# Kernel tuning notes

Measured on AMD Instinct MI355X. Metric: run time of the kernel, lower is better.

Reference implementation:

```python
import jax, jax.numpy as jnp
import numpy as np
from jax import lax

BATCH = 32; SEQ_LEN = 336; ENC_IN = 7; MARK_IN = 4
D_MODEL = 512; D_FF = 2048; N_HEADS = 8; DK = 64; DV = 64
E_LAYERS = 3; D_BOTTLE = 128; PRED_LEN = 96
WINDOW = (4, 4, 4); INNER = 5


def _mask_sizes():
    # Pyraformer get_mask: True = masked out
    all_size = [SEQ_LEN]
    for w in WINDOW:
        all_size.append(all_size[-1] // w)
    S = sum(all_size)
    m = np.zeros((S, S), bool)  # True = may attend
    iw = INNER // 2
    starts = np.cumsum([0] + all_size)
    for l, sz in enumerate(all_size):
        st = int(starts[l])
        for i in range(st, st + sz):
            m[i, max(i - iw, st):min(i + iw + 1, st + sz)] = True
    for l in range(1, len(all_size)):
        st = int(starts[l])
        for i in range(st, st + all_size[l]):
            left = (st - all_size[l - 1]) + (i - st) * WINDOW[l - 1]
            right = st if i == st + all_size[l] - 1 else (st - all_size[l - 1]) + (i - st + 1) * WINDOW[l - 1]
            m[i, left:right] = True
            m[left:right, i] = True
    return ~m, all_size


def _refer_points(all_size):
    idx = np.zeros((all_size[0], len(all_size)), np.int64)
    for i in range(all_size[0]):
        idx[i, 0] = i
        former = i
        for j in range(1, len(all_size)):
            start = sum(all_size[:j])
            inner = former - (start - all_size[j - 1])
            former = start + min(inner // WINDOW[j - 1], all_size[j] - 1)
            idx[i, j] = former
    return idx


def _pos_enc(L, d):
    pos = np.arange(L)[:, None].astype(np.float32)
    div = np.exp(np.arange(0, d, 2).astype(np.float32) * (-np.log(10000.0) / d))
    pe = np.zeros((L, d), np.float32)
    pe[:, 0::2] = np.sin(pos * div)
    pe[:, 1::2] = np.cos(pos * div)
    return pe


def _ln(x, g, b, eps=1e-5):
    mu = jnp.mean(x, -1, keepdims=True)
    v = jnp.mean((x - mu) ** 2, -1, keepdims=True)
    return (x - mu) * lax.rsqrt(v + eps) * g + b


def setup_inputs():
    key = jax.random.key(0)
    ks = iter(jax.random.split(key, 64))
    def nrm(shape, s=0.02):
        return jax.random.normal(next(ks), shape, jnp.float32) * s
    mask, all_size = _mask_sizes()
    inp = {
        "x_enc": jax.random.normal(next(ks), (BATCH, SEQ_LEN, ENC_IN), jnp.float32),
        "x_mark_enc": jax.random.normal(next(ks), (BATCH, SEQ_LEN, MARK_IN), jnp.float32),
        "x_dec": jax.random.normal(next(ks), (BATCH, PRED_LEN, ENC_IN), jnp.float32),
        "x_mark_dec": jax.random.normal(next(ks), (BATCH, PRED_LEN, MARK_IN), jnp.float32),
        "conv_embed_w": nrm((D_MODEL, ENC_IN, 3), 0.1),
        "time_w": nrm((MARK_IN, D_MODEL)),
        "time_b": jnp.zeros((D_MODEL,), jnp.float32),
        "down_w": nrm((D_MODEL, D_BOTTLE)),
        "down_b": jnp.zeros((D_BOTTLE,), jnp.float32),
        "cscm_conv_w": nrm((3, D_BOTTLE, D_BOTTLE, 4), 0.05),
        "cscm_conv_b": jnp.zeros((3, D_BOTTLE), jnp.float32),
        "bn_g": jnp.ones((3, D_BOTTLE), jnp.float32),
        "bn_b": jnp.zeros((3, D_BOTTLE), jnp.float32),
        "up_w": nrm((D_BOTTLE, D_MODEL)),
        "up_b": jnp.zeros((D_MODEL,), jnp.float32),
        "cscm_ln_g": jnp.ones((D_MODEL,), jnp.float32),
        "cscm_ln_b": jnp.zeros((D_MODEL,), jnp.float32),
        "wq": nrm((E_LAYERS, D_MODEL, N_HEADS * DK)),
        "wk": nrm((E_LAYERS, D_MODEL, N_HEADS * DK)),
        "wv": nrm((E_LAYERS, D_MODEL, N_HEADS * DV)),
        "wo": nrm((E_LAYERS, N_HEADS * DV, D_MODEL)),
        "ln1_g": jnp.ones((E_LAYERS, D_MODEL), jnp.float32),
        "ln1_b": jnp.zeros((E_LAYERS, D_MODEL), jnp.float32),
        "ffn_w1": nrm((E_LAYERS, D_MODEL, D_FF)),
        "ffn_b1": jnp.zeros((E_LAYERS, D_FF), jnp.float32),
        "ffn_w2": nrm((E_LAYERS, D_FF, D_MODEL)),
        "ffn_b2": jnp.zeros((E_LAYERS, D_MODEL), jnp.float32),
        "ln2_g": jnp.ones((E_LAYERS, D_MODEL), jnp.float32),
        "ln2_b": jnp.zeros((E_LAYERS, D_MODEL), jnp.float32),
        "pred_w": nrm((len(all_size) * D_MODEL, PRED_LEN * ENC_IN)),
        "attn_mask": jnp.asarray(mask),                 # [S,S] bool, True = masked
        "indexes": jnp.asarray(_refer_points(all_size)),  # [336, 4] int64
    }
    return inp


def _forward(x_enc, x_mark_enc, conv_embed_w, time_w, time_b, down_w, down_b,
             cscm_conv_w, cscm_conv_b, bn_g, bn_b, up_w, up_b, cscm_ln_g, cscm_ln_b,
             wq, wk, wv, wo, ln1_g, ln1_b, ffn_w1, ffn_b1, ffn_w2, ffn_b2, ln2_g, ln2_b,
             pred_w, attn_mask, indexes):
    B = x_enc.shape[0]
    dn = ('NWC', 'OIW', 'NWC')
    # DataEmbedding: circular conv1d token embedding + sinusoidal pos + linear time-feature embedding
    xp = jnp.concatenate([x_enc[:, -1:], x_enc, x_enc[:, :1]], axis=1)  # circular pad, k=3
    tok = lax.conv_general_dilated(xp, conv_embed_w, (1,), 'VALID', dimension_numbers=dn)
    pe = jnp.asarray(_pos_enc(SEQ_LEN, D_MODEL))
    emb = tok + pe[None] + x_mark_enc @ time_w + time_b  # [B,336,512]
    # Bottleneck_Construct (CSCM): down-proj, strided convs per scale, up-proj, concat, LN
    x = emb @ down_w + down_b  # [B,336,128]
    outs = []
    for i in range(len(WINDOW)):
        x = lax.conv_general_dilated(x, cscm_conv_w[i], (WINDOW[i],), 'VALID', dimension_numbers=dn) + cscm_conv_b[i]
        x = x * bn_g[i] + bn_b[i]  # eval-mode BatchNorm1d (running mean 0 / var 1)
        x = jax.nn.elu(x)
        outs.append(x)  # lengths 84, 21, 5
    coarse = jnp.concatenate(outs, axis=1) @ up_w + up_b  # [B,110,512]
    seq = _ln(jnp.concatenate([emb, coarse], axis=1), cscm_ln_g, cscm_ln_b)  # [B,446,512]
    S = seq.shape[1]
    neg = jnp.where(attn_mask, jnp.float32(-1e9), jnp.float32(0.0))  # [S,S]
    scale = 1.0 / np.sqrt(DK).astype(np.float32)
    for l in range(E_LAYERS):  # post-norm encoder layers
        q = (seq @ wq[l]).reshape(B, S, N_HEADS, DK)
        k = (seq @ wk[l]).reshape(B, S, N_HEADS, DK)
        v = (seq @ wv[l]).reshape(B, S, N_HEADS, DV)
        attn = jax.nn.softmax(jnp.einsum('bihd,bjhd->bhij', q, k) * scale + neg, axis=-1)
        o = jnp.einsum('bhij,bjhd->bihd', attn, v).reshape(B, S, N_HEADS * DV)
        seq = _ln(seq + o @ wo[l], ln1_g[l], ln1_b[l])
        h = jax.nn.gelu(seq @ ffn_w1[l] + ffn_b1[l], approximate=False)
        seq = _ln(seq + h @ ffn_w2[l] + ffn_b2[l], ln2_g[l], ln2_b[l])
    # pyramidal readout: gather each scale's ancestor node for every fine position
    g = seq[:, indexes.reshape(-1), :].reshape(B, SEQ_LEN, -1)  # [B,336,4*512]
    enc_out = g[:, -1, :]  # [B,2048]
    return (enc_out @ pred_w).reshape(B, PRED_LEN, ENC_IN)


def reference(x_enc, x_mark_enc, x_dec, x_mark_dec, conv_embed_w, time_w, time_b,
              down_w, down_b, cscm_conv_w, cscm_conv_b, bn_g, bn_b, up_w, up_b,
              cscm_ln_g, cscm_ln_b, wq, wk, wv, wo, ln1_g, ln1_b, ffn_w1, ffn_b1,
              ffn_w2, ffn_b2, ln2_g, ln2_b, pred_w, attn_mask, indexes):
    # x_dec / x_mark_dec are unused by Pyraformer's forward (kept for signature parity)
    return _forward(x_enc, x_mark_enc, conv_embed_w, time_w, time_b, down_w, down_b,
                    cscm_conv_w, cscm_conv_b, bn_g, bn_b, up_w, up_b, cscm_ln_g, cscm_ln_b,
                    wq, wk, wv, wo, ln1_g, ln1_b, ffn_w1, ffn_b1, ffn_w2, ffn_b2,
                    ln2_g, ln2_b, pred_w, attn_mask, indexes)
```

## Files before the change

kernel.cpp:

```cpp
#include <hip/hip_runtime.h>
#include <math.h>

constexpr int BB   = 32;
constexpr int L    = 336;
constexpr int CIN  = 7;
constexpr int MARK = 4;
constexpr int D    = 512;
constexpr int DFF  = 2048;
constexpr int NH   = 8;
constexpr int HD   = 64;
constexpr int S    = 446;
constexpr int DBOT = 128;
constexpr int L1 = 84, L2 = 21, L3 = 5;
constexpr int LC = 110;
constexpr int NLAYER = 3;
constexpr int PRED_N = 672;
constexpr int MP   = 14336;
constexpr int NMAX = 12;
constexpr int MCONV1 = BB * L1;
constexpr int MCONV2P = 768;
constexpr int MCAT  = 3584;

using short8  = __attribute__((ext_vector_type(8))) short;
using float4v = __attribute__((ext_vector_type(4))) float;

struct SetsData {
    int nbr[S][NMAX];
    int idx[4][S];
    int cnt[4];
};

constexpr SetsData compute_sets() {
    SetsData sd{};
    constexpr int sizes[4]  = {336, 84, 21, 5};
    constexpr int starts[4] = {0, 336, 420, 441};
    for (int i = 0; i < S; ++i) {
        int li = 0, pi = i;
        if (i < 336)      { li = 0; pi = i; }
        else if (i < 420) { li = 1; pi = i - 336; }
        else if (i < 441) { li = 2; pi = i - 420; }
        else              { li = 3; pi = i - 441; }
        int cnt = 0;
        for (int d = -2; d <= 2; ++d) {
            int q = pi + d;
            if (q >= 0 && q < sizes[li]) sd.nbr[i][cnt++] = starts[li] + q;
        }
        if (li > 0) {
            int lo = pi * 4;
            int hi = (pi == sizes[li] - 1) ? sizes[li - 1] : (pi + 1) * 4;
            for (int c = lo; c < hi; ++c) sd.nbr[i][cnt++] = starts[li - 1] + c;
        }
        if (li < 3) {
            int q = pi >> 2;
            if (q > sizes[li + 1] - 1) q = sizes[li + 1] - 1;
            sd.nbr[i][cnt++] = starts[li + 1] + q;
        }
        for (int j = cnt; j < NMAX; ++j) sd.nbr[i][j] = -1;
    }
    sd.cnt[3] = 4;
    sd.idx[3][0] = 335; sd.idx[3][1] = 419; sd.idx[3][2] = 440; sd.idx[3][3] = 445;
    for (int lvl = 3; lvl >= 1; --lvl) {
        bool mk[S] = {};
        for (int k = 0; k < sd.cnt[lvl]; ++k) {
            int i = sd.idx[lvl][k];
            for (int t = 0; t < NMAX; ++t) {
                int v = sd.nbr[i][t];
                if (v >= 0) mk[v] = true;
            }
        }
        int nc = 0;
        for (int i = 0; i < S; ++i)
            if (mk[i]) sd.idx[lvl - 1][nc++] = i;
        sd.cnt[lvl - 1] = nc;
    }
    return sd;
}

constexpr SetsData HS = compute_sets();
__constant__ SetsData d_sets = compute_sets();

constexpr size_t psk_elems() {
    size_t mx = 0;
    for (int l = 0; l < NLAYER; ++l) {
        size_t Mc = (size_t)HS.cnt[l + 1] * 32;
        size_t Mpad = ((Mc + 127) / 128) * 128;
        if (Mc <= 512) { size_t v = 4 * Mpad * 512;  if (v > mx) mx = v; }
        if (Mc <= 128) { size_t v = 4 * Mpad * 2048; if (v > mx) mx = v; }
        size_t ks = (Mc <= 512) ? 8 : 4;
        size_t v = ks * Mpad * 512; if (v > mx) mx = v;
    }
    return mx;
}

__device__ inline short f2bf(float f) {
    union { float f; unsigned u; } v; v.f = f;
    unsigned r = v.u + 0x7fffu + ((v.u >> 16) & 1u);
    return (short)(r >> 16);
}
__device__ inline float bf2f(short h) {
    union { unsigned u; float f; } v; v.u = ((unsigned)(unsigned short)h) << 16;
    return v.f;
}

__device__ inline void gload_lds16(const void* g, void* l) {
    __builtin_amdgcn_global_load_lds(
        (const __attribute__((address_space(1))) void*)g,
        (__attribute__((address_space(3))) void*)l, 16, 0, 0);
}


template<int EPI>
__launch_bounds__(256, 4)
__global__ void mfma_gemm(const short* __restrict__ A, const short* __restrict__ Bt,
                          const float* __restrict__ bias, const float* __restrict__ bias2,
                          void* __restrict__ Cout, int Kd, int Nd,
                          int alvl, int clvl, int cnt,
                          const float* __restrict__ peT, short* __restrict__ Cout2) {
    __shared__ short As[2][128 * 32];
    __shared__ short Bs[2][128 * 32];
    int tid = threadIdx.x;
    int nwg  = gridDim.x * gridDim.y;
    int orig = blockIdx.y * gridDim.x + blockIdx.x;
    int qq = nwg >> 3, rr = nwg & 7;
    int xcd = orig & 7, idx = orig >> 3;
    int wgid = (xcd < rr ? xcd * (qq + 1) : rr * (qq + 1) + (xcd - rr) * qq) + idx;
    int m0 = (wgid / gridDim.x) * 128, n0 = (wgid % gridDim.x) * 128;

    int lane = tid & 63, wid = tid >> 6;
    int wm = wid >> 1, wn = wid & 1;
    int lr = lane & 15, lk = lane >> 4;

    size_t abase[2], bbase[2];
#pragma unroll
    for (int r = 0; r < 2; ++r) {
        int u = r * 256 + tid;
        int row = ((u >> 3) << 1) | ((u >> 2) & 1);
        int kg  = (u & 3) ^ ((u >> 3) & 3);
        int rm = m0 + row, ga;
        if (alvl >= 0) { int j = rm >> 5; if (j > cnt - 1) j = cnt - 1; ga = (rm & 31) * S + d_sets.idx[alvl][j]; }
        else ga = rm;
        abase[r] = (size_t)ga * Kd + kg * 8;
        bbase[r] = (size_t)(n0 + row) * Kd + kg * 8;
    }
    auto stage = [&](int buf, int k0) {
#pragma unroll
        for (int r = 0; r < 2; ++r) {
            short* la = As[buf] + (size_t)(r * 256 + wid * 64) * 8;
            short* lb = Bs[buf] + (size_t)(r * 256 + wid * 64) * 8;
            gload_lds16(A + abase[r] + k0, la);
            gload_lds16(Bt + bbase[r] + k0, lb);
        }
    };
    auto rd_off = [&](int row_) {
        int rh = row_ >> 1;
        int s  = lk ^ (rh & 3);
        return (size_t)(rh * 8 + (row_ & 1) * 4 + s) * 8;
    };

    float4v acc[4][4];
#pragma unroll
    for (int i = 0; i < 4; ++i)
#pragma unroll
        for (int j = 0; j < 4; ++j) acc[i][j] = 0;

    const int nt = Kd >> 5;
    stage(0, 0);
    for (int t = 0; t < nt; ++t) {
        int cur = t & 1;
        if (t + 1 < nt) {
            stage(cur ^ 1, (t + 1) * 32);
            asm volatile("s_waitcnt vmcnt(4)" ::: "memory");
        } else {
            asm volatile("s_waitcnt vmcnt(0)" ::: "memory");
        }
        __builtin_amdgcn_s_barrier();
        short8 af[4], bfv[4];
#pragma unroll
        for (int mi = 0; mi < 4; ++mi)
            af[mi] = *(const short8*)(As[cur] + rd_off(wm * 64 + mi * 16 + lr));
#pragma unroll
        for (int ni = 0; ni < 4; ++ni)
            bfv[ni] = *(const short8*)(Bs[cur] + rd_off(wn * 64 + ni * 16 + lr));
        __builtin_amdgcn_s_setprio(1);
#pragma unroll
        for (int mi = 0; mi < 4; ++mi)
#pragma unroll
            for (int ni = 0; ni < 4; ++ni)
                acc[mi][ni] = __builtin_amdgcn_mfma_f32_16x16x32_bf16(
                    af[mi], bfv[ni], acc[mi][ni], 0, 0, 0);
        __builtin_amdgcn_s_setprio(0);
        __builtin_amdgcn_s_barrier();
    }

#pragma unroll
    for (int mi = 0; mi < 4; ++mi) {
        int gmc = m0 + wm * 64 + mi * 16 + lk * 4;
#pragma unroll
        for (int ni = 0; ni < 4; ++ni) {
            int gn = n0 + wn * 64 + ni * 16 + lr;
            float bsv = (EPI == 1 || EPI == 3 || EPI == 4) ? bias[gn] : 0.0f;
            float sc = (EPI == 5) ? bias[gn]  : 0.0f;
            float sh = (EPI == 5) ? bias2[gn] : 0.0f;
#pragma unroll
            for (int e = 0; e < 4; ++e) {
                int rm = gmc + e, grow;
                if (clvl >= 0) { int j = rm >> 5; if (j > cnt - 1) j = cnt - 1; grow = (rm & 31) * S + d_sets.idx[clvl][j]; }
                else grow = rm;
                float v = acc[mi][ni][e] + bsv;
                if (EPI == 3) v = 0.5f * v * (1.0f + erff(v * 0.70710678118654752f));
                if (EPI == 5) { v = v * sc + sh; v = v > 0.0f ? v : (expf(v) - 1.0f); }
                if (EPI == 6) {
                    v += peT[(size_t)(grow % L) * D + gn];
                    ((float*)Cout)[(size_t)grow * Nd + gn] = v;
                    Cout2[(size_t)grow * Nd + gn] = f2bf(v);
                } else if (EPI <= 1) {
                    ((float*)Cout)[(size_t)grow * Nd + gn] = v;
                } else {
                    ((short*)Cout)[(size_t)grow * Nd + gn] = f2bf(v);
                }
            }
        }
    }
}

__launch_bounds__(256, 4)
__global__ void mfma_gemm_sk(const short* __restrict__ A, const short* __restrict__ Bt,
                             float* __restrict__ part, int Kd, int Nd,
                             int alvl, int cnt) {
    __shared__ short As[2][128 * 32];
    __shared__ short Bs[2][128 * 32];
    int tid = threadIdx.x;
    int nwg  = gridDim.x * gridDim.y;
    int orig = blockIdx.y * gridDim.x + blockIdx.x;
    int qq = nwg >> 3, rr = nwg & 7;
    int xcd = orig & 7, idx = orig >> 3;
    int wgid = (xcd < rr ? xcd * (qq + 1) : rr * (qq + 1) + (xcd - rr) * qq) + idx;
    int m0 = (wgid / gridDim.x) * 128, n0 = (wgid % gridDim.x) * 128;
    int Mpad = gridDim.y * 128;
    int kz = blockIdx.z;
    int kb = Kd / gridDim.z;
    int kbase = kz * kb;

    int lane = tid & 63, wid = tid >> 6;
    int wm = wid >> 1, wn = wid & 1;
    int lr = lane & 15, lk = lane >> 4;

    size_t abase[2], bbase[2];
#pragma unroll
    for (int r = 0; r < 2; ++r) {
        int u = r * 256 + tid;
        int row = ((u >> 3) << 1) | ((u >> 2) & 1);
        int kg  = (u & 3) ^ ((u >> 3) & 3);
        int rm = m0 + row, ga;
        if (alvl >= 0) { int j = rm >> 5; if (j > cnt - 1) j = cnt - 1; ga = (rm & 31) * S + d_sets.idx[alvl][j]; }
        else ga = rm;
        abase[r] = (size_t)ga * Kd + kbase + kg * 8;
        bbase[r] = (size_t)(n0 + row) * Kd + kbase + kg * 8;
    }
    auto stage = [&](int buf, int k0) {
#pragma unroll
        for (int r = 0; r < 2; ++r) {
            short* la = As[buf] + (size_t)(r * 256 + wid * 64) * 8;
            short* lb = Bs[buf] + (size_t)(r * 256 + wid * 64) * 8;
            gload_lds16(A + abase[r] + k0, la);
            gload_lds16(Bt + bbase[r] + k0, lb);
        }
    };
    auto rd_off = [&](int row_) {
        int rh = row_ >> 1;
        int s  = lk ^ (rh & 3);
        return (size_t)(rh * 8 + (row_ & 1) * 4 + s) * 8;
    };

    float4v acc[4][4];
#pragma unroll
    for (int i = 0; i < 4; ++i)
#pragma unroll
        for (int j = 0; j < 4; ++j) acc[i][j] = 0;

    const int nt = kb >> 5;
    stage(0, 0);
    for (int t = 0; t < nt; ++t) {
        int cur = t & 1;
        if (t + 1 < nt) {
            stage(cur ^ 1, (t + 1) * 32);
            asm volatile("s_waitcnt vmcnt(4)" ::: "memory");
        } else {
            asm volatile("s_waitcnt vmcnt(0)" ::: "memory");
        }
        __builtin_amdgcn_s_barrier();
        short8 af[4], bfv[4];
#pragma unroll
        for (int mi = 0; mi < 4; ++mi)
            af[mi] = *(const short8*)(As[cur] + rd_off(wm * 64 + mi * 16 + lr));
#pragma unroll
        for (int ni = 0; ni < 4; ++ni)
            bfv[ni] = *(const short8*)(Bs[cur] + rd_off(wn * 64 + ni * 16 + lr));
        __builtin_amdgcn_s_setprio(1);
#pragma unroll
        for (int mi = 0; mi < 4; ++mi)
#pragma unroll
            for (int ni = 0; ni < 4; ++ni)
                acc[mi][ni] = __builtin_amdgcn_mfma_f32_16x16x32_bf16(
                    af[mi], bfv[ni], acc[mi][ni], 0, 0, 0);
        __builtin_amdgcn_s_setprio(0);
        __builtin_amdgcn_s_barrier();
    }

#pragma unroll
    for (int mi = 0; mi < 4; ++mi) {
        int gmc = m0 + wm * 64 + mi * 16 + lk * 4;
#pragma unroll
        for (int ni = 0; ni < 4; ++ni) {
            int gn = n0 + wn * 64 + ni * 16 + lr;
#pragma unroll
            for (int e = 0; e < 4; ++e)
                part[((size_t)kz * Mpad + gmc + e) * Nd + gn] = acc[mi][ni][e];
        }
    }
}

template<int EPI>
__launch_bounds__(256)
__global__ void reduce_sk(const float* __restrict__ part, const float* __restrict__ bias,
                          short* __restrict__ Cout, int Mpad, int Nd, int KS) {
    int idx = blockIdx.x * 256 + threadIdx.x;
    if (idx >= Mpad * Nd) return;
    float s = 0.0f;
    for (int k = 0; k < KS; ++k)
        s += part[(size_t)k * Mpad * Nd + idx];
    if (EPI == 3 || EPI == 4) s += bias[idx % Nd];
    if (EPI == 3) s = 0.5f * s * (1.0f + erff(s * 0.70710678118654752f));
    Cout[idx] = f2bf(s);
}

__device__ inline void wtrans_tile(const float* __restrict__ W, short* __restrict__ Wt,
                                   int Kd, int Nd, int n0, int k0, int tid) {
    __shared__ float tile[32][33];
    int tx = tid & 31, ty = tid >> 5;
#pragma unroll
    for (int r = 0; r < 32; r += 8)
        tile[ty + r][tx] = W[(size_t)(k0 + ty + r) * Nd + n0 + tx];
    __syncthreads();
#pragma unroll
    for (int r = 0; r < 32; r += 8)
        Wt[(size_t)(n0 + ty + r) * Kd + k0 + tx] = f2bf(tile[tx][ty + r]);
}

__launch_bounds__(256)
__global__ void wtrans_qkvo(const float* __restrict__ wq, const float* __restrict__ wk,
                            const float* __restrict__ wv, const float* __restrict__ wo,
                            short* __restrict__ wqkvT, short* __restrict__ woT) {
    int z = blockIdx.z, l = z >> 2, part = z & 3;
    const float* src = (part == 0 ? wq : part == 1 ? wk : part == 2 ? wv : wo)
                       + (size_t)l * D * D;
    short* dst = (part < 3) ? wqkvT + (size_t)l * 3 * D * D + (size_t)part * D * D
                            : woT + (size_t)l * D * D;
    wtrans_tile(src, dst, D, D, blockIdx.x * 32, blockIdx.y * 32, threadIdx.x);
}

__launch_bounds__(256)
__global__ void wtrans_ffn(const float* __restrict__ w1, const float* __restrict__ w2,
                           short* __restrict__ w1T, short* __restrict__ w2T) {
    int z = blockIdx.z, l = z >> 1, part = z & 1;
    int nt = part ? blockIdx.y : blockIdx.x;
    int kt = part ? blockIdx.x : blockIdx.y;
    if (part == 0)
        wtrans_tile(w1 + (size_t)l * D * DFF, w1T + (size_t)l * DFF * D,
                    D, DFF, nt * 32, kt * 32, threadIdx.x);
    else
        wtrans_tile(w2 + (size_t)l * DFF * D, w2T + (size_t)l * D * DFF,
                    DFF, D, nt * 32, kt * 32, threadIdx.x);
}

__launch_bounds__(256)
__global__ void wtrans_small(const float* __restrict__ down_w, short* __restrict__ downT,
                             const float* __restrict__ up_w, short* __restrict__ upT,
                             const float* __restrict__ cw, const float* __restrict__ cb,
                             const float* __restrict__ bg, const float* __restrict__ bb,
                             short* __restrict__ cscmT, float* __restrict__ sc,
                             float* __restrict__ sh) {
    int b = blockIdx.x;
    if (b < 64) {
        wtrans_tile(down_w, downT, D, DBOT, (b & 3) * 32, (b >> 2) * 32, threadIdx.x);
    } else if (b < 128) {
        int b2 = b - 64;
        wtrans_tile(up_w, upT, DBOT, D, (b2 & 15) * 32, (b2 >> 4) * 32, threadIdx.x);
    } else {
        int idx = (b - 128) * 256 + threadIdx.x;
        if (idx < 2 * DBOT * 512) {
            int l = idx >> 16;
            int rem = idx & 65535;
            int oc = rem >> 9, j = rem & 511;
            int r = j >> 7, c = j & 127;
            cscmT[idx] = f2bf(cw[(((size_t)l * DBOT + oc) * DBOT + c) * 4 + r]);
        }
        if (idx < 3 * DBOT) {
            sc[idx] = bg[idx];
            sh[idx] = cb[idx] * bg[idx] + bb[idx];
        }
    }
}

constexpr int PE_N  = L * D;
constexpr int WE_N  = D * 32;
constexpr int XIM_N = BB * L * 32;
constexpr int MISC_N = PE_N + WE_N + XIM_N;

__launch_bounds__(256)
__global__ void prep_misc(const float* __restrict__ x_enc, const float* __restrict__ x_mark,
                          const float* __restrict__ cw, const float* __restrict__ tw,
                          const float* __restrict__ tb, float* __restrict__ pe,
                          short* __restrict__ wE, short* __restrict__ xim) {
    int idx = blockIdx.x * 256 + threadIdx.x;
    if (idx < PE_N) {
        int d = idx % D, t = idx / D;
        int e = d & ~1;
        float div = expf(-(float)e * (logf(10000.0f) / (float)D));
        float arg = (float)t * div;
        pe[idx] = (d & 1) ? cosf(arg) : sinf(arg);
        return;
    }
    int i2 = idx - PE_N;
    if (i2 < WE_N) {
        int k = i2 & 31, d = i2 >> 5;
        float v = 0.0f;
        if (k < 21) {
            int w = k / 7, i = k % 7;
            v = cw[(size_t)d * (CIN * 3) + i * 3 + w];
        } else if (k < 25) {
            v = tw[(size_t)(k - 21) * D + d];
        } else if (k == 25) {
            v = tb[d];
        }
        wE[i2] = f2bf(v);
        return;
    }
    int i3 = i2 - WE_N;
    if (i3 < XIM_N) {
        int k = i3 & 31, m = i3 >> 5;
        int t = m % L, b = m / L;
        float v = 0.0f;
        if (k < 21) {
            int w = k / 7, i = k % 7;
            int s = t + w - 1;
            if (s < 0) s = L - 1;
            if (s >= L) s = 0;
            v = x_enc[((size_t)b * L + s) * CIN + i];
        } else if (k < 25) {
            v = x_mark[(size_t)m * MARK + (k - 21)];
        } else if (k == 25) {
            v = 1.0f;
        }
        xim[i3] = f2bf(v);
    }
}

__launch_bounds__(128)
__global__ void cscm_conv_bf16(const short* __restrict__ in, int inRowsPerB,
                               short* __restrict__ outp, const float* __restrict__ w,
                               const float* __restrict__ cb, const float* __restrict__ bng,
                               const float* __restrict__ bnb, int Lout) {
    int bid = blockIdx.x;
    int to = bid % Lout, b = bid / Lout;
    __shared__ float insh[4 * DBOT];
    int tid = threadIdx.x;
#pragma unroll
    for (int r = 0; r < 4; ++r)
        insh[r * DBOT + tid] = bf2f(in[((size_t)(b * inRowsPerB + to * 4 + r)) * DBOT + tid]);
    __syncthreads();
    float acc = cb[tid];
    const float* wr = w + (size_t)tid * (DBOT * 4);
    for (int c = 0; c < DBOT; ++c) {
#pragma unroll
        for (int r = 0; r < 4; ++r)
            acc += insh[r * DBOT + c] * wr[c * 4 + r];
    }
    acc = acc * bng[tid] + bnb[tid];
    outp[((size_t)(b * Lout + to)) * DBOT + tid] = f2bf(acc > 0.0f ? acc : (expf(acc) - 1.0f));
}

__launch_bounds__(256)
__global__ void concat_cs_kernel(const short* __restrict__ cs1, const short* __restrict__ cs2,
                                 const short* __restrict__ cs3, short* __restrict__ csc) {
    int idx = blockIdx.x * 256 + threadIdx.x;
    if (idx >= MCAT * DBOT) return;
    int m = idx >> 7, c = idx & 127;
    short v = 0;
    if (m < BB * LC) {
        int b = m / LC, t = m % LC;
        if (t < L1)           v = cs1[(size_t)(b * L1 + t) * DBOT + c];
        else if (t < L1 + L2) v = cs2[(size_t)(b * L2 + (t - L1)) * DBOT + c];
        else                  v = cs3[(size_t)(b * L3 + (t - L1 - L2)) * DBOT + c];
    }
    csc[idx] = v;
}

__launch_bounds__(256)
__global__ void attn_sparse_kernel(const short* __restrict__ QKV, short* __restrict__ Ob,
                                   int lvl, int cnt) {
    int wid  = blockIdx.x * 4 + (threadIdx.x >> 6);
    if (wid >= cnt * 32) return;
    int lane = threadIdx.x & 63;
    int b = wid & 31, j = wid >> 5;
    int i = d_sets.idx[lvl][j];
    const short8 qv = *(const short8*)(QKV + (size_t)(b * S + i) * 1536 + lane * 8);
    float qf[8];
#pragma unroll
    for (int e = 0; e < 8; ++e) qf[e] = bf2f(qv[e]);
    int nb[NMAX];
#pragma unroll
    for (int jj = 0; jj < NMAX; ++jj) nb[jj] = d_sets.nbr[i][jj];
    float sc[NMAX];
#pragma unroll
    for (int jj = 0; jj < NMAX; ++jj) {
        float s = -1e30f;
        if (nb[jj] >= 0) {
            const short8 kv = *(const short8*)(QKV + (size_t)(b * S + nb[jj]) * 1536 + 512 + lane * 8);
            s = 0.0f;
#pragma unroll
            for (int e = 0; e < 8; ++e) s += qf[e] * bf2f(kv[e]);
            s += __shfl_xor(s, 1); s += __shfl_xor(s, 2); s += __shfl_xor(s, 4);
            s *= 0.125f;
        }
        sc[jj] = s;
    }
    float mx = sc[0];
#pragma unroll
    for (int jj = 1; jj < NMAX; ++jj) mx = fmaxf(mx, sc[jj]);
    float sum = 0.0f;
    float accv[8] = {};
#pragma unroll
    for (int jj = 0; jj < NMAX; ++jj) {
        float p = expf(sc[jj] - mx);
        sum += p;
        if (nb[jj] >= 0) {
            const short8 vv = *(const short8*)(QKV + (size_t)(b * S + nb[jj]) * 1536 + 1024 + lane * 8);
#pragma unroll
            for (int e = 0; e < 8; ++e) accv[e] += p * bf2f(vv[e]);
        }
    }
    float inv = 1.0f / sum;
    short8 ov;
#pragma unroll
    for (int e = 0; e < 8; ++e) ov[e] = f2bf(accv[e] * inv);
    *(short8*)(Ob + (size_t)wid * D + lane * 8) = ov;
}

__device__ inline float blk_reduce(float v, float* ws4, int tid) {
#pragma unroll
    for (int o = 32; o; o >>= 1) v += __shfl_xor(v, o);
    if ((tid & 63) == 0) ws4[tid >> 6] = v;
    __syncthreads();
    return ws4[0] + ws4[1] + ws4[2] + ws4[3];
}

__launch_bounds__(256)
__global__ void concat_ln_idx(const float* __restrict__ emb, const float* __restrict__ coarse,
                              const float* __restrict__ g, const float* __restrict__ bta,
                              float* __restrict__ seq, short* __restrict__ seq_bf) {
    int row = blockIdx.x;
    int b = row & 31, j = row >> 5;
    int s = d_sets.idx[0][j];
    int orig = b * S + s;
    const float* src = (s < L) ? emb + ((size_t)b * L + s) * D
                               : coarse + ((size_t)b * LC + (s - L)) * D;
    __shared__ float wsA[4];
    __shared__ float wsB[4];
    int tid = threadIdx.x;
    float x0 = src[tid], x1 = src[tid + 256];
    float mu = blk_reduce(x0 + x1, wsA, tid) * (1.0f / D);
    float d0 = x0 - mu, d1 = x1 - mu;
    float var = blk_reduce(d0 * d0 + d1 * d1, wsB, tid) * (1.0f / D);
    float rstd = rsqrtf(var + 1e-5f);
    float v0 = d0 * rstd * g[tid]       + bta[tid];
    float v1 = d1 * rstd * g[tid + 256] + bta[tid + 256];
    float* dst = seq + (size_t)orig * D;
    dst[tid] = v0; dst[tid + 256] = v1;
    short* dbf = seq_bf + (size_t)orig * D;
    dbf[tid] = f2bf(v0); dbf[tid + 256] = f2bf(v1);
}

__launch_bounds__(256)
__global__ void add_ln_idx(float* __restrict__ seq, const short* __restrict__ add,
                           const float* __restrict__ g, const float* __restrict__ bta,
                           short* __restrict__ seq_bf, int lvl) {
    int row = blockIdx.x;
    int b = row & 31, j = row >> 5;
    int orig = b * S + d_sets.idx[lvl][j];
    __shared__ float wsA[4];
    __shared__ float wsB[4];
    int tid = threadIdx.x;
    float* srow = seq + (size_t)orig * D;
    const short* arow = add + (size_t)row * D;
    float x0 = srow[tid] + bf2f(arow[tid]);
    float x1 = srow[tid + 256] + bf2f(arow[tid + 256]);
    float mu = blk_reduce(x0 + x1, wsA, tid) * (1.0f / D);
    float d0 = x0 - mu, d1 = x1 - mu;
    float var = blk_reduce(d0 * d0 + d1 * d1, wsB, tid) * (1.0f / D);
    float rstd = rsqrtf(var + 1e-5f);
    float v0 = d0 * rstd * g[tid]       + bta[tid];
    float v1 = d1 * rstd * g[tid + 256] + bta[tid + 256];
    srow[tid] = v0; srow[tid + 256] = v1;
    short* dbf = seq_bf + (size_t)orig * D;
    dbf[tid] = f2bf(v0); dbf[tid + 256] = f2bf(v1);
}

__launch_bounds__(256)
__global__ void add_ln_sk(float* __restrict__ seq, const float* __restrict__ part,
                          const float* __restrict__ bias, const float* __restrict__ g,
                          const float* __restrict__ bta, short* __restrict__ seq_bf,
                          int lvl, int Mpad, int KS) {
    int row = blockIdx.x;
    int b = row & 31, j = row >> 5;
    int orig = b * S + d_sets.idx[lvl][j];
    __shared__ float wsA[4];
    __shared__ float wsB[4];
    int tid = threadIdx.x;
    float a0 = 0.0f, a1 = 0.0f;
    for (int k = 0; k < KS; ++k) {
        const float* pr = part + ((size_t)k * Mpad + row) * D;
        a0 += pr[tid];
        a1 += pr[tid + 256];
    }
    if (bias) { a0 += bias[tid]; a1 += bias[tid + 256]; }
    float* srow = seq + (size_t)orig * D;
    float x0 = srow[tid] + a0;
    float x1 = srow[tid + 256] + a1;
    float mu = blk_reduce(x0 + x1, wsA, tid) * (1.0f / D);
    float d0 = x0 - mu, d1 = x1 - mu;
    float var = blk_reduce(d0 * d0 + d1 * d1, wsB, tid) * (1.0f / D);
    float rstd = rsqrtf(var + 1e-5f);
    float v0 = d0 * rstd * g[tid]       + bta[tid];
    float v1 = d1 * rstd * g[tid + 256] + bta[tid + 256];
    srow[tid] = v0; srow[tid + 256] = v1;
    short* dbf = seq_bf + (size_t)orig * D;
    dbf[tid] = f2bf(v0); dbf[tid + 256] = f2bf(v1);
}

__launch_bounds__(256)
__global__ void pred_kernel(const float* __restrict__ seq, const float* __restrict__ w,
                            float* __restrict__ part) {
    __shared__ float es[32][257];
    __shared__ float wsm[256][8];
    int tid = threadIdx.x;
    int n0 = blockIdx.x * 8;
    int ks = blockIdx.y;
    int k0 = ks * 256;
    const int pos[4] = {335, 419, 440, 445};
    int seg = ks >> 1;
    int dbase = (ks & 1) * 256;
#pragma unroll 8
    for (int r = 0; r < 32; ++r)
        es[r][tid] = seq[((size_t)r * S + pos[seg]) * D + dbase + tid];
#pragma unroll
    for (int e = 0; e < 8; ++e)
        wsm[tid][e] = w[(size_t)(k0 + tid) * PRED_N + n0 + e];
    __syncthreads();
    int b = tid >> 3, nn = tid & 7;
    float acc = 0.0f;
#pragma unroll 8
    for (int kk = 0; kk < 256; ++kk)
        acc += es[b][kk] * wsm[kk][nn];
    part[(size_t)ks * (BB * PRED_N) + (size_t)b * PRED_N + n0 + nn] = acc;
}

__launch_bounds__(256)
__global__ void pred_reduce_kernel(const float* __restrict__ part, float* __restrict__ out) {
    int idx = blockIdx.x * 256 + threadIdx.x;
    if (idx >= BB * PRED_N) return;
    float s = 0.0f;
#pragma unroll
    for (int k = 0; k < 8; ++k) s += part[(size_t)k * (BB * PRED_N) + idx];
    out[idx] = s;
}

extern "C" void kernel_launch(void* const* d_in, const int* in_sizes, int n_in,
                              void* d_out, int out_size, void* d_ws, size_t ws_size,
                              hipStream_t stream) {
    const float* x_enc      = (const float*)d_in[0];
    const float* x_mark_enc = (const float*)d_in[1];
    const float* conv_embed_w = (const float*)d_in[4];
    const float* time_w  = (const float*)d_in[5];
    const float* time_b  = (const float*)d_in[6];
    const float* down_w  = (const float*)d_in[7];
    const float* down_b  = (const float*)d_in[8];
    const float* cscm_w  = (const float*)d_in[9];
    const float* cscm_b  = (const float*)d_in[10];
    const float* bn_g    = (const float*)d_in[11];
    const float* bn_b    = (const float*)d_in[12];
    const float* up_w    = (const float*)d_in[13];
    const float* up_b    = (const float*)d_in[14];
    const float* cln_g   = (const float*)d_in[15];
    const float* cln_b   = (const float*)d_in[16];
    const float* wq      = (const float*)d_in[17];
    const float* wk      = (const float*)d_in[18];
    const float* wv      = (const float*)d_in[19];
    const float* wo      = (const float*)d_in[20];
    const float* ln1_g   = (const float*)d_in[21];
    const float* ln1_b   = (const float*)d_in[22];
    const float* ffn_w1  = (const float*)d_in[23];
    const float* ffn_b1  = (const float*)d_in[24];
    const float* ffn_w2  = (const float*)d_in[25];
    const float* ffn_b2  = (const float*)d_in[26];
    const float* ln2_g   = (const float*)d_in[27];
    const float* ln2_b   = (const float*)d_in[28];
    const float* pred_w  = (const float*)d_in[29];
    float* out = (float*)d_out;

    char* w8 = (char*)d_ws;
    size_t off = 0;
    auto alloc = [&](size_t bytes) {
        void* p = w8 + off;
        off = (off + bytes + 255) & ~(size_t)255;
        return p;
    };
    float* emb    = (float*)alloc((size_t)BB * L * D * 4);
    short* emb_bf = (short*)alloc((size_t)BB * L * D * 2);
    float* pe     = (float*)alloc((size_t)L * D * 4);
    short* xim    = (short*)alloc((size_t)BB * L * 32 * 2);
    short* wE     = (short*)alloc((size_t)D * 32 * 2);
    short* xd_bf  = (short*)alloc((size_t)BB * L * DBOT * 2);
    short* cs1_bf = (short*)alloc((size_t)MCONV2P * 512 * 2);
    short* cs2_bf = (short*)alloc((size_t)MCONV2P * DBOT * 2);
    short* cs3_bf = (short*)alloc((size_t)BB * L3 * DBOT * 2);
    short* csc_bf = (short*)alloc((size_t)MCAT * DBOT * 2);
    float* coarse = (float*)alloc((size_t)MCAT * D * 4);
    float* seq    = (float*)alloc((size_t)BB * S * D * 4);
    short* T1     = (short*)alloc((size_t)MP * D * 2);
    float* part   = (float*)alloc((size_t)8 * BB * PRED_N * 4);
    float* partsk = (float*)alloc(psk_elems() * 4);
    short* seq_bf = (short*)alloc((size_t)MP * D * 2);
    short* QKV    = (short*)alloc((size_t)MP * 3 * D * 2);
    short* Ob     = (short*)alloc((size_t)MP * D * 2);
    short* hidden = QKV;
    short* wqkvT  = (short*)alloc((size_t)NLAYER * 3 * D * D * 2);
    short* woT    = (short*)alloc((size_t)NLAYER * D * D * 2);
    short* w1T    = (short*)alloc((size_t)NLAYER * DFF * D * 2);
    short* w2T    = (short*)alloc((size_t)NLAYER * D * DFF * 2);
    short* downT  = (short*)alloc((size_t)DBOT * D * 2);
    short* upT    = (short*)alloc((size_t)D * DBOT * 2);
    short* cscmT  = (short*)alloc((size_t)2 * DBOT * 512 * 2);
    float* csc_sc = (float*)alloc((size_t)3 * DBOT * 4);
    float* csc_sh = (float*)alloc((size_t)3 * DBOT * 4);
    (void)ws_size; (void)in_sizes; (void)n_in; (void)out_size;

    const int rowsL = BB * L;
    dim3 blk(256);

    wtrans_qkvo<<<dim3(16, 16, 4 * NLAYER), blk, 0, stream>>>(wq, wk, wv, wo, wqkvT, woT);
    wtrans_ffn<<<dim3(64, 16, 2 * NLAYER), blk, 0, stream>>>(ffn_w1, ffn_w2, w1T, w2T);
    wtrans_small<<<dim3(128 + 512), blk, 0, stream>>>(
        down_w, downT, up_w, upT, cscm_w, cscm_b, bn_g, bn_b, cscmT, csc_sc, csc_sh);
    prep_misc<<<dim3((MISC_N + 255) / 256), blk, 0, stream>>>(
        x_enc, x_mark_enc, conv_embed_w, time_w, time_b, pe, wE, xim);
    mfma_gemm<6><<<dim3(D / 128, rowsL / 128), blk, 0, stream>>>(
        xim, wE, nullptr, nullptr, emb, 32, D, -1, -1, 0, pe, emb_bf);
    mfma_gemm<4><<<dim3(1, rowsL / 128), blk, 0, stream>>>(
        emb_bf, downT, down_b, nullptr, xd_bf, D, DBOT, -1, -1, 0, nullptr, nullptr);
    mfma_gemm<5><<<dim3(1, MCONV1 / 128), blk, 0, stream>>>(
        xd_bf, cscmT, csc_sc, csc_sh, cs1_bf, 512, DBOT, -1, -1, 0, nullptr, nullptr);
    mfma_gemm<5><<<dim3(1, MCONV2P / 128), blk, 0, stream>>>(
        cs1_bf, cscmT + (size_t)DBOT * 512, csc_sc + DBOT, csc_sh + DBOT,
        cs2_bf, 512, DBOT, -1, -1, 0, nullptr, nullptr);
    cscm_conv_bf16<<<dim3(BB * L3), dim3(DBOT), 0, stream>>>(
        cs2_bf, L2, cs3_bf, cscm_w + 2 * DBOT * DBOT * 4,
        cscm_b + 2 * DBOT, bn_g + 2 * DBOT, bn_b + 2 * DBOT, L3);
    concat_cs_kernel<<<dim3((MCAT * DBOT + 255) / 256), blk, 0, stream>>>(
        cs1_bf, cs2_bf, cs3_bf, csc_bf);
    mfma_gemm<1><<<dim3(D / 128, MCAT / 128), blk, 0, stream>>>(
        csc_bf, upT, up_b, nullptr, coarse, DBOT, D, -1, -1, 0, nullptr, nullptr);
    concat_ln_idx<<<dim3(HS.cnt[0] * 32), blk, 0, stream>>>(
        emb, coarse, cln_g, cln_b, seq, seq_bf);

    for (int l = 0; l < NLAYER; ++l) {
        const int inLvl = l, outLvl = l + 1;
        const int inCnt  = HS.cnt[l];
        const int outCnt = HS.cnt[l + 1];
        const int Mc   = outCnt * 32;
        const int Mpad = ((Mc + 127) / 128) * 128;
        mfma_gemm<2><<<dim3(3 * D / 128, (inCnt * 32 + 127) / 128), blk, 0, stream>>>(
            seq_bf, wqkvT + (size_t)l * 3 * D * D, nullptr, nullptr, QKV, D, 3 * D,
            inLvl, inLvl, inCnt, nullptr, nullptr);
        attn_sparse_kernel<<<dim3(outCnt * 8), blk, 0, stream>>>(
            QKV, Ob, outLvl, outCnt);
        if (Mc <= 512) {
            mfma_gemm_sk<<<dim3(D / 128, Mpad / 128, 4), blk, 0, stream>>>(
                Ob, woT + (size_t)l * D * D, partsk, D, D, -1, 0);
            add_ln_sk<<<dim3(Mc), blk, 0, stream>>>(
                seq, partsk, nullptr, ln1_g + (size_t)l * D, ln1_b + (size_t)l * D,
                seq_bf, outLvl, Mpad, 4);
        } else {
            mfma_gemm<2><<<dim3(D / 128, Mpad / 128), blk, 0, stream>>>(
                Ob, woT + (size_t)l * D * D, nullptr, nullptr, T1, D, D,
                -1, -1, 0, nullptr, nullptr);
            add_ln_idx<<<dim3(Mc), blk, 0, stream>>>(
                seq, T1, ln1_g + (size_t)l * D, ln1_b + (size_t)l * D, seq_bf, outLvl);
        }
        if (Mc <= 128) {
            mfma_gemm_sk<<<dim3(DFF / 128, Mpad / 128, 4), blk, 0, stream>>>(
                seq_bf, w1T + (size_t)l * DFF * D, partsk, D, DFF, outLvl, outCnt);
            reduce_sk<3><<<dim3((Mpad * DFF + 255) / 256), blk, 0, stream>>>(
                partsk, ffn_b1 + (size_t)l * DFF, hidden, Mpad, DFF, 4);
        } else {
            mfma_gemm<3><<<dim3(DFF / 128, Mpad / 128), blk, 0, stream>>>(
                seq_bf, w1T + (size_t)l * DFF * D, ffn_b1 + (size_t)l * DFF, nullptr,
                hidden, D, DFF, outLvl, -1, outCnt, nullptr, nullptr);
        }
        {
            int KS = (Mc <= 512) ? 8 : 4;
            mfma_gemm_sk<<<dim3(D / 128, Mpad / 128, KS), blk, 0, stream>>>(
                hidden, w2T + (size_t)l * D * DFF, partsk, DFF, D, -1, 0);
            add_ln_sk<<<dim3(Mc), blk, 0, stream>>>(
                seq, partsk, ffn_b2 + (size_t)l * D, ln2_g + (size_t)l * D,
                ln2_b + (size_t)l * D, seq_bf, outLvl, Mpad, KS);
        }
    }

    pred_kernel<<<dim3(PRED_N / 8, 8), blk, 0, stream>>>(seq, pred_w, part);
    pred_reduce_kernel<<<dim3((BB * PRED_N + 255) / 256), blk, 0, stream>>>(part, out);
}
```

Before: 360.4 us.

## Split-K the narrow CSCM GEMMs and drop the fp32 embedding buffer

The down-projection and the two CSCM conv GEMMs each have only one 128-wide N tile, so they launch few blocks. They now run as 4-way split-K GEMMs, with a reduce kernel that applies the bias, or the BN scale/shift and ELU epilogue. The fp32 copy of the embedding output is no longer written; the concat/LayerNorm reads the bf16 copy instead. This adds kernel launches and fp32 partial-sum traffic through global memory, and the LayerNorm input for fine positions now has bf16 precision.

```diff
diff --git a/kernel.cpp b/kernel.cpp
--- a/kernel.cpp
+++ b/kernel.cpp
@@ -80,7 +80,11 @@
 __constant__ SetsData d_sets = compute_sets();
 
 constexpr size_t psk_elems() {
-    size_t mx = 0;
+    size_t mx = 4 * (size_t)BB * L * DBOT;
+    {
+        size_t v = 4 * (size_t)MCONV1 * DBOT; if (v > mx) mx = v;
+        v = 4 * (size_t)MCONV2P * DBOT;       if (v > mx) mx = v;
+    }
     for (int l = 0; l < NLAYER; ++l) {
         size_t Mc = (size_t)HS.cnt[l + 1] * 32;
         size_t Mpad = ((Mc + 127) / 128) * 128;
@@ -211,7 +215,6 @@
                 if (EPI == 5) { v = v * sc + sh; v = v > 0.0f ? v : (expf(v) - 1.0f); }
                 if (EPI == 6) {
                     v += peT[(size_t)(grow % L) * D + gn];
-                    ((float*)Cout)[(size_t)grow * Nd + gn] = v;
                     Cout2[(size_t)grow * Nd + gn] = f2bf(v);
                 } else if (EPI <= 1) {
                     ((float*)Cout)[(size_t)grow * Nd + gn] = v;
@@ -323,14 +326,17 @@
 template<int EPI>
 __launch_bounds__(256)
 __global__ void reduce_sk(const float* __restrict__ part, const float* __restrict__ bias,
-                          short* __restrict__ Cout, int Mpad, int Nd, int KS) {
+                          const float* __restrict__ bias2, short* __restrict__ Cout,
+                          int Mpad, int Nd, int KS) {
     int idx = blockIdx.x * 256 + threadIdx.x;
     if (idx >= Mpad * Nd) return;
     float s = 0.0f;
     for (int k = 0; k < KS; ++k)
         s += part[(size_t)k * Mpad * Nd + idx];
-    if (EPI == 3 || EPI == 4) s += bias[idx % Nd];
+    int n = idx % Nd;
+    if (EPI == 3 || EPI == 4) s += bias[n];
     if (EPI == 3) s = 0.5f * s * (1.0f + erff(s * 0.70710678118654752f));
+    if (EPI == 5) { s = s * bias[n] + bias2[n]; s = s > 0.0f ? s : (expf(s) - 1.0f); }
     Cout[idx] = f2bf(s);
 }
 
@@ -556,19 +562,24 @@
 }
 
 __launch_bounds__(256)
-__global__ void concat_ln_idx(const float* __restrict__ emb, const float* __restrict__ coarse,
+__global__ void concat_ln_idx(const short* __restrict__ emb_bf, const float* __restrict__ coarse,
                               const float* __restrict__ g, const float* __restrict__ bta,
                               float* __restrict__ seq, short* __restrict__ seq_bf) {
     int row = blockIdx.x;
     int b = row & 31, j = row >> 5;
     int s = d_sets.idx[0][j];
     int orig = b * S + s;
-    const float* src = (s < L) ? emb + ((size_t)b * L + s) * D
-                               : coarse + ((size_t)b * LC + (s - L)) * D;
     __shared__ float wsA[4];
     __shared__ float wsB[4];
     int tid = threadIdx.x;
-    float x0 = src[tid], x1 = src[tid + 256];
+    float x0, x1;
+    if (s < L) {
+        const short* src = emb_bf + ((size_t)b * L + s) * D;
+        x0 = bf2f(src[tid]); x1 = bf2f(src[tid + 256]);
+    } else {
+        const float* src = coarse + ((size_t)b * LC + (s - L)) * D;
+        x0 = src[tid]; x1 = src[tid + 256];
+    }
     float mu = blk_reduce(x0 + x1, wsA, tid) * (1.0f / D);
     float d0 = x0 - mu, d1 = x1 - mu;
     float var = blk_reduce(d0 * d0 + d1 * d1, wsB, tid) * (1.0f / D);
@@ -715,7 +726,6 @@
         off = (off + bytes + 255) & ~(size_t)255;
         return p;
     };
-    float* emb    = (float*)alloc((size_t)BB * L * D * 4);
     short* emb_bf = (short*)alloc((size_t)BB * L * D * 2);
     float* pe     = (float*)alloc((size_t)L * D * 4);
     short* xim    = (short*)alloc((size_t)BB * L * 32 * 2);
@@ -755,14 +765,19 @@
     prep_misc<<<dim3((MISC_N + 255) / 256), blk, 0, stream>>>(
         x_enc, x_mark_enc, conv_embed_w, time_w, time_b, pe, wE, xim);
     mfma_gemm<6><<<dim3(D / 128, rowsL / 128), blk, 0, stream>>>(
-        xim, wE, nullptr, nullptr, emb, 32, D, -1, -1, 0, pe, emb_bf);
-    mfma_gemm<4><<<dim3(1, rowsL / 128), blk, 0, stream>>>(
-        emb_bf, downT, down_b, nullptr, xd_bf, D, DBOT, -1, -1, 0, nullptr, nullptr);
-    mfma_gemm<5><<<dim3(1, MCONV1 / 128), blk, 0, stream>>>(
-        xd_bf, cscmT, csc_sc, csc_sh, cs1_bf, 512, DBOT, -1, -1, 0, nullptr, nullptr);
-    mfma_gemm<5><<<dim3(1, MCONV2P / 128), blk, 0, stream>>>(
-        cs1_bf, cscmT + (size_t)DBOT * 512, csc_sc + DBOT, csc_sh + DBOT,
-        cs2_bf, 512, DBOT, -1, -1, 0, nullptr, nullptr);
+        xim, wE, nullptr, nullptr, nullptr, 32, D, -1, -1, 0, pe, emb_bf);
+    mfma_gemm_sk<<<dim3(1, rowsL / 128, 4), blk, 0, stream>>>(
+        emb_bf, downT, partsk, D, DBOT, -1, 0);
+    reduce_sk<4><<<dim3((rowsL * DBOT + 255) / 256), blk, 0, stream>>>(
+        partsk, down_b, nullptr, xd_bf, rowsL, DBOT, 4);
+    mfma_gemm_sk<<<dim3(1, MCONV1 / 128, 4), blk, 0, stream>>>(
+        xd_bf, cscmT, partsk, 512, DBOT, -1, 0);
+    reduce_sk<5><<<dim3((MCONV1 * DBOT + 255) / 256), blk, 0, stream>>>(
+        partsk, csc_sc, csc_sh, cs1_bf, MCONV1, DBOT, 4);
+    mfma_gemm_sk<<<dim3(1, MCONV2P / 128, 4), blk, 0, stream>>>(
+        cs1_bf, cscmT + (size_t)DBOT * 512, partsk, 512, DBOT, -1, 0);
+    reduce_sk<5><<<dim3((MCONV2P * DBOT + 255) / 256), blk, 0, stream>>>(
+        partsk, csc_sc + DBOT, csc_sh + DBOT, cs2_bf, MCONV2P, DBOT, 4);
     cscm_conv_bf16<<<dim3(BB * L3), dim3(DBOT), 0, stream>>>(
         cs2_bf, L2, cs3_bf, cscm_w + 2 * DBOT * DBOT * 4,
         cscm_b + 2 * DBOT, bn_g + 2 * DBOT, bn_b + 2 * DBOT, L3);
@@ -771,7 +786,7 @@
     mfma_gemm<1><<<dim3(D / 128, MCAT / 128), blk, 0, stream>>>(
         csc_bf, upT, up_b, nullptr, coarse, DBOT, D, -1, -1, 0, nullptr, nullptr);
     concat_ln_idx<<<dim3(HS.cnt[0] * 32), blk, 0, stream>>>(
-        emb, coarse, cln_g, cln_b, seq, seq_bf);
+        emb_bf, coarse, cln_g, cln_b, seq, seq_bf);
 
     for (int l = 0; l < NLAYER; ++l) {
         const int inLvl = l, outLvl = l + 1;
@@ -801,7 +816,7 @@
             mfma_gemm_sk<<<dim3(DFF / 128, Mpad / 128, 4), blk, 0, stream>>>(
                 seq_bf, w1T + (size_t)l * DFF * D, partsk, D, DFF, outLvl, outCnt);
             reduce_sk<3><<<dim3((Mpad * DFF + 255) / 256), blk, 0, stream>>>(
-                partsk, ffn_b1 + (size_t)l * DFF, hidden, Mpad, DFF, 4);
+                partsk, ffn_b1 + (size_t)l * DFF, nullptr, hidden, Mpad, DFF, 4);
         } else {
             mfma_gemm<3><<<dim3(DFF / 128, Mpad / 128), blk, 0, stream>>>(
                 seq_bf, w1T + (size_t)l * DFF * D, ffn_b1 + (size_t)l * DFF, nullptr,
```

After: 347.1 us. 1.04x faster.
